# Kernel tuning notes

Measured on AMD Instinct MI355X. Metric: run time of the kernel, lower is better.

Reference implementation:

```python
import jax, jax.numpy as jnp
import numpy as np

HEAD_SIZE = 64
N_EMBD = 1024
BLOCK_SIZE = 2048


def setup_inputs() -> dict:
    key = jax.random.key(0)
    ks = jax.random.split(key, 7)
    B, T = 4, 2048
    s = 1.0 / np.sqrt(N_EMBD)
    return {
        "x": jax.random.normal(ks[0], (B, T, N_EMBD), dtype=jnp.float32),
        "Wq": jax.random.normal(ks[1], (N_EMBD, HEAD_SIZE), dtype=jnp.float32) * s,
        "bq": jnp.zeros((HEAD_SIZE,), dtype=jnp.float32),
        "Wk": jax.random.normal(ks[2], (N_EMBD, HEAD_SIZE), dtype=jnp.float32) * s,
        "bk": jnp.zeros((HEAD_SIZE,), dtype=jnp.float32),
        "Wv": jax.random.normal(ks[3], (N_EMBD, HEAD_SIZE), dtype=jnp.float32) * s,
        "bv": jnp.zeros((HEAD_SIZE,), dtype=jnp.float32),
    }


def reference(x, Wq, bq, Wk, bk, Wv, bv):
    # x: [B, T, n_embd]
    B, T, _ = x.shape
    q = x @ Wq + bq  # [B, T, H]
    k = x @ Wk + bk
    v = x @ Wv + bv
    # Faithful to source: divides by head_size**(-0.5) == multiplies by sqrt(head_size)
    scale = jnp.float32(HEAD_SIZE) ** 0.5
    scores = jnp.einsum("bqh,bkh->bqk", q, k) * scale  # [B, T, T]
    causal = jnp.tril(jnp.ones((T, T), dtype=bool))
    scores = jnp.where(causal, scores, -jnp.inf)
    attn = jax.nn.softmax(scores, axis=-1)  # dropout p=0.0 (eval)
    out = jnp.einsum("bqk,bkh->bqh", attn, v)  # [B, T, H]
    return out
```

## Files before the change

kernel.cpp:

```cpp
#include <hip/hip_runtime.h>
#include <math.h>

#define NE 1024
#define HS 64
#define TT 2048
#define QSC 11.541560327111707f

typedef __bf16    v8bf __attribute__((ext_vector_type(8)));
typedef _Float16  v8h  __attribute__((ext_vector_type(8)));
typedef float     v4f  __attribute__((ext_vector_type(4)));

#define MFMA_BF(a, b, c)  __builtin_amdgcn_mfma_f32_16x16x32_bf16((a), (b), (c), 0, 0, 0)
#define MFMA_F16(a, b, c) __builtin_amdgcn_mfma_f32_16x16x32_f16((a), (b), (c), 0, 0, 0)

__device__ __forceinline__ void gl_lds16(const void* g, void* l) {
    __builtin_amdgcn_global_load_lds(
        (const __attribute__((address_space(1))) unsigned int*)g,
        (__attribute__((address_space(3))) unsigned int*)l, 16, 0, 0);
}
__device__ __forceinline__ void gl_lds4(const void* g, void* l) {
    __builtin_amdgcn_global_load_lds(
        (const __attribute__((address_space(1))) unsigned int*)g,
        (__attribute__((address_space(3))) unsigned int*)l, 4, 0, 0);
}

#define SYNC_VM(imm) do {                                   \
    __asm__ __volatile__("" ::: "memory");                  \
    __builtin_amdgcn_s_waitcnt(imm);                        \
    __builtin_amdgcn_s_barrier();                           \
    __asm__ __volatile__("" ::: "memory");                  \
} while (0)
#define WAIT_VM8  0x0F78
#define WAIT_VM0  0x0F70

__global__ __launch_bounds__(256) void prep_w(
    const float* __restrict__ Wq, const float* __restrict__ Wk,
    const float* __restrict__ Wv, char* __restrict__ imgW)
{
    __shared__ float t[64][65];
    const int bx = blockIdx.x, by = blockIdx.y;
    const float* W = (by == 0) ? Wq : ((by == 1) ? Wk : Wv);
    const int tid = threadIdx.x;
    const int cc = tid & 63, r4 = tid >> 6;
    #pragma unroll
    for (int p = 0; p < 16; ++p) {
        const int k = p * 4 + r4;
        t[k][cc] = W[(size_t)(bx * 64 + k) * HS + cc];
    }
    __syncthreads();
    #pragma unroll
    for (int e = 0; e < 4; ++e) {
        const int chunk = tid + e * 256;
        const int s2   = chunk >> 9;
        const int rem  = chunk & 511;
        const int ctl  = rem >> 7;
        const int rem2 = rem & 127;
        const int pl   = rem2 >> 6;
        const int rem3 = rem2 & 63;
        const int c    = rem3 >> 2;
        const int p16  = rem3 & 3;
        const int kb   = s2 * 32 + ((p16 ^ (c & 3)) << 3);
        const int ncol = ctl * 16 + c;
        v8bf o;
        #pragma unroll
        for (int j = 0; j < 8; ++j) {
            const float v = t[kb + j][ncol];
            const __bf16 h = (__bf16)v;
            o[j] = pl ? (__bf16)(v - (float)h) : h;
        }
        *(v8bf*)(imgW + (size_t)(bx * 2 + s2) * 24576
                 + (by * 4 + ctl) * 2048 + pl * 1024 + c * 64 + p16 * 16) = o;
    }
}

__global__ __launch_bounds__(256, 2) void proj(
    const float* __restrict__ x, const char* __restrict__ imgW,
    const float* __restrict__ bq, const float* __restrict__ bk,
    const float* __restrict__ bv,
    _Float16* __restrict__ qh, _Float16* __restrict__ ql,
    _Float16* __restrict__ kf, _Float16* __restrict__ vt)
{
    __shared__ __align__(16) char sbuf[3][26624];

    const int tid = threadIdx.x, lane = tid & 63, cg = tid >> 6;
    const int quad = lane >> 4, l16 = lane & 15;
    const int m0 = blockIdx.x * 16;

    const int wv = cg;
    const int xr0 = wv * 4 + (lane >> 5);
    const int xr1 = xr0 + 2;
    const int xp  = (lane >> 3) & 3;
    const int xj  = lane & 7;
    const float* gx0 = x + (size_t)(m0 + xr0) * NE + ((xp ^ (xr0 & 3)) << 3) + xj;
    const float* gx1 = x + (size_t)(m0 + xr1) * NE + ((xp ^ (xr1 & 3)) << 3) + xj;
    const int xl0 = wv * 512 + (lane & 63) * 4;
    const int xl1 = xl0 + 256;
    const char* gw = imgW + (size_t)tid * 16;

    v4f acc[3];
    #pragma unroll
    for (int i = 0; i < 3; ++i) acc[i] = (v4f){0.f, 0.f, 0.f, 0.f};

    #define STAGE(ks, xb_)  do {                                          \
        gl_lds4(gx0 + (ks) * 32, (xb_) + xl0);                            \
        gl_lds4(gx1 + (ks) * 32, (xb_) + xl1);                            \
        const char* gws_ = gw + (size_t)(ks) * 24576;                     \
        _Pragma("unroll")                                                 \
        for (int j_ = 0; j_ < 6; ++j_)                                    \
            gl_lds16(gws_ + j_ * 4096, (xb_) + 2048 + tid * 16 + j_ * 4096); \
    } while (0)

    auto compute = [&](int ks) {
        const char* xb = sbuf[ks % 3];
        const char* wb = xb + 2048;
        const int rl = l16;
        const int pA = quad ^ (rl & 3);
        const float4 a0 = *(const float4*)(xb + rl * 128 + pA * 32);
        const float4 a1 = *(const float4*)(xb + rl * 128 + pA * 32 + 16);
        const float av[8] = {a0.x, a0.y, a0.z, a0.w, a1.x, a1.y, a1.z, a1.w};
        v8bf ah, al;
        #pragma unroll
        for (int i = 0; i < 8; ++i) {
            const __bf16 h = (__bf16)av[i];
            ah[i] = h;
            al[i] = (__bf16)(av[i] - (float)h);
        }
        const int wo = l16 * 64 + ((quad ^ (l16 & 3)) << 4);
        #pragma unroll
        for (int j = 0; j < 3; ++j) {
            const char* base = wb + (cg * 3 + j) * 2048 + wo;
            const v8bf bh = *(const v8bf*)(base);
            const v8bf bl = *(const v8bf*)(base + 1024);
            acc[j] = MFMA_BF(ah, bh, acc[j]);
            acc[j] = MFMA_BF(ah, bl, acc[j]);
            acc[j] = MFMA_BF(al, bh, acc[j]);
        }
    };

    STAGE(0, sbuf[0]);
    STAGE(1, sbuf[1]);
    for (int ks = 0; ks < 31; ++ks) {
        SYNC_VM(WAIT_VM8);
        if (ks + 2 < 32) STAGE(ks + 2, sbuf[(ks + 2) % 3]);
        compute(ks);
    }
    SYNC_VM(WAIT_VM0);
    compute(31);
    #undef STAGE

    #pragma unroll
    for (int j = 0; j < 3; ++j) {
        const int n = cg * 48 + j * 16 + l16;
        const float bias = (n < 64) ? bq[n] : ((n < 128) ? bk[n - 64] : bv[n - 128]);
        #pragma unroll
        for (int reg = 0; reg < 4; ++reg) {
            const int row = m0 + quad * 4 + reg;
            const float v = acc[j][reg] + bias;
            if (n < 64) {
                const float s = v * QSC;
                const _Float16 hh = (_Float16)s;
                qh[(size_t)row * HS + n] = hh;
                ql[(size_t)row * HS + n] = (_Float16)(s - (float)hh);
            } else if (n < 128) {
                kf[(size_t)row * HS + n - 64] = (_Float16)v;
            } else {
                const int b2 = row >> 11, tt = row & 2047, hc = n - 128;
                vt[((size_t)(b2 * HS + hc)) * TT + tt] = (_Float16)v;
            }
        }
    }
}

__global__ __launch_bounds__(512, 2) void attn(
    const _Float16* __restrict__ qh, const _Float16* __restrict__ ql,
    const _Float16* __restrict__ kf, const _Float16* __restrict__ vt,
    float* __restrict__ out)
{
    __shared__ __align__(16) char smem_raw[69632];
    _Float16* ps = (_Float16*)smem_raw;
    float*    os = (float*)smem_raw;
    __shared__ float sm[8][2][16], sl[8][2][16];

    const int tid = threadIdx.x, lane = tid & 63, w = tid >> 6;
    const int quad = lane >> 4, l16 = lane & 15;
    const int b = blockIdx.x & 3, pair = blockIdx.x >> 2;
    const int q0t[2] = {(127 - pair) * 16, pair * 16};
    const int ntk0 = (q0t[0] + 16 + 63) >> 6;
    const int ntk1 = (q0t[1] + 16 + 63) >> 6;
    const int total = ntk0 + ntk1;

    v8h Qh0[2], Qh1[2], Ql0[2], Ql1[2];
    #pragma unroll
    for (int t = 0; t < 2; ++t) {
        const size_t qrow = ((size_t)b * TT + q0t[t] + l16) * HS;
        Qh0[t] = *(const v8h*)(qh + qrow + quad * 8);
        Qh1[t] = *(const v8h*)(qh + qrow + 32 + quad * 8);
        Ql0[t] = *(const v8h*)(ql + qrow + quad * 8);
        Ql1[t] = *(const v8h*)(ql + qrow + 32 + quad * 8);
    }

    const v8h vones = {(_Float16)1.f, (_Float16)1.f, (_Float16)1.f, (_Float16)1.f,
                       (_Float16)1.f, (_Float16)1.f, (_Float16)1.f, (_Float16)1.f};

    float mr0[4] = {-3e38f, -3e38f, -3e38f, -3e38f};
    float mr1[4] = {-3e38f, -3e38f, -3e38f, -3e38f};
    v4f o0[4], o1[4], l40, l41;
    #pragma unroll
    for (int i = 0; i < 4; ++i) {
        o0[i] = (v4f){0.f, 0.f, 0.f, 0.f};
        o1[i] = (v4f){0.f, 0.f, 0.f, 0.f};
    }
    l40 = (v4f){0.f, 0.f, 0.f, 0.f};
    l41 = (v4f){0.f, 0.f, 0.f, 0.f};

    _Float16* pw = ps + w * (16 * 72);

    auto doChunk = [&](int j0, int q0c, int t,
                       float (&mrow)[4], v4f (&o)[4], v4f &o4) {
        v8h Kf[8], Vf[8];
        #pragma unroll
        for (int nt = 0; nt < 4; ++nt) {
            const size_t krow = ((size_t)b * TT + j0 + nt * 16 + l16) * HS;
            Kf[nt * 2]     = *(const v8h*)(kf + krow + quad * 8);
            Kf[nt * 2 + 1] = *(const v8h*)(kf + krow + 32 + quad * 8);
        }
        #pragma unroll
        for (int nt = 0; nt < 4; ++nt) {
            const size_t vrow = ((size_t)(b * HS + nt * 16 + l16)) * TT + j0;
            Vf[nt * 2]     = *(const v8h*)(vt + vrow + quad * 8);
            Vf[nt * 2 + 1] = *(const v8h*)(vt + vrow + 32 + quad * 8);
        }
        v4f s[4];
        #pragma unroll
        for (int i = 0; i < 4; ++i) s[i] = (v4f){0.f, 0.f, 0.f, 0.f};
        #pragma unroll
        for (int nt = 0; nt < 4; ++nt) {
            s[nt] = MFMA_F16(Qh0[t], Kf[nt * 2],     s[nt]);
            s[nt] = MFMA_F16(Qh1[t], Kf[nt * 2 + 1], s[nt]);
            s[nt] = MFMA_F16(Ql0[t], Kf[nt * 2],     s[nt]);
            s[nt] = MFMA_F16(Ql1[t], Kf[nt * 2 + 1], s[nt]);
        }
        const int irow = q0c + quad * 4;
        float mx[4] = {-3e38f, -3e38f, -3e38f, -3e38f};
        #pragma unroll
        for (int nt = 0; nt < 4; ++nt)
            #pragma unroll
            for (int reg = 0; reg < 4; ++reg) {
                if (j0 + nt * 16 + l16 > irow + reg) s[nt][reg] = -3e38f;
                mx[reg] = fmaxf(mx[reg], s[nt][reg]);
            }
        #pragma unroll
        for (int off = 8; off; off >>= 1)
            #pragma unroll
            for (int reg = 0; reg < 4; ++reg)
                mx[reg] = fmaxf(mx[reg], __shfl_xor(mx[reg], off));
        float al[4];
        #pragma unroll
        for (int reg = 0; reg < 4; ++reg) {
            const float mn = fmaxf(mrow[reg], mx[reg]);
            al[reg] = exp2f(mrow[reg] - mn);
            mrow[reg] = mn;
        }
        #pragma unroll
        for (int nt = 0; nt < 4; ++nt)
            #pragma unroll
            for (int reg = 0; reg < 4; ++reg) {
                const float p = (j0 + nt * 16 + l16 > irow + reg)
                                    ? 0.f : exp2f(s[nt][reg] - mrow[reg]);
                pw[(quad * 4 + reg) * 72 + nt * 16 + l16] = (_Float16)p;
            }
        #pragma unroll
        for (int nt = 0; nt < 4; ++nt)
            #pragma unroll
            for (int reg = 0; reg < 4; ++reg)
                o[nt][reg] *= al[reg];
        #pragma unroll
        for (int reg = 0; reg < 4; ++reg)
            o4[reg] *= al[reg];
        const v8h Pa0 = *(const v8h*)(pw + l16 * 72 + quad * 8);
        const v8h Pa1 = *(const v8h*)(pw + l16 * 72 + 32 + quad * 8);
        #pragma unroll
        for (int nt = 0; nt < 4; ++nt) {
            o[nt] = MFMA_F16(Pa0, Vf[nt * 2],     o[nt]);
            o[nt] = MFMA_F16(Pa1, Vf[nt * 2 + 1], o[nt]);
        }
        o4 = MFMA_F16(Pa0, vones, o4);
        o4 = MFMA_F16(Pa1, vones, o4);
    };

    for (int c = w; c < total; c += 8) {
        if (c < ntk0) doChunk(c * 64,          q0t[0], 0, mr0, o0, l40);
        else          doChunk((c - ntk0) * 64, q0t[1], 1, mr1, o1, l41);
    }

    if (l16 == 0) {
        #pragma unroll
        for (int reg = 0; reg < 4; ++reg) {
            sm[w][0][quad * 4 + reg] = mr0[reg];
            sl[w][0][quad * 4 + reg] = l40[reg];
            sm[w][1][quad * 4 + reg] = mr1[reg];
            sl[w][1][quad * 4 + reg] = l41[reg];
        }
    }
    __syncthreads();

    #pragma unroll
    for (int t = 0; t < 2; ++t) {
        float sc[4];
        #pragma unroll
        for (int reg = 0; reg < 4; ++reg) {
            const int r = quad * 4 + reg;
            float M = sm[0][t][r];
            #pragma unroll
            for (int i = 1; i < 8; ++i) M = fmaxf(M, sm[i][t][r]);
            const float mw = t ? mr1[reg] : mr0[reg];
            sc[reg] = exp2f(mw - M);
        }
        float* ow = os + (size_t)(w * 2 + t) * (16 * 68);
        #pragma unroll
        for (int nt = 0; nt < 4; ++nt)
            #pragma unroll
            for (int reg = 0; reg < 4; ++reg) {
                const v4f& oo = t ? o1[nt] : o0[nt];
                ow[(quad * 4 + reg) * 68 + nt * 16 + l16] = oo[reg] * sc[reg];
            }
    }
    __syncthreads();

    #pragma unroll
    for (int kk = 0; kk < 4; ++kk) {
        const int g = w * 4 + kk;
        const int t = g >> 4, m = g & 15;
        float M = sm[0][t][m];
        #pragma unroll
        for (int i = 1; i < 8; ++i) M = fmaxf(M, sm[i][t][m]);
        float L = 0.f, val = 0.f;
        #pragma unroll
        for (int i = 0; i < 8; ++i) {
            L   += sl[i][t][m] * exp2f(sm[i][t][m] - M);
            val += os[(size_t)(i * 2 + t) * (16 * 68) + m * 68 + lane];
        }
        out[((size_t)b * TT + q0t[t] + m) * HS + lane] = val / L;
    }
}

extern "C" void kernel_launch(void* const* d_in, const int* in_sizes, int n_in,
                              void* d_out, int out_size, void* d_ws, size_t ws_size,
                              hipStream_t stream)
{
    const float* x  = (const float*)d_in[0];
    const float* Wq = (const float*)d_in[1];
    const float* bq = (const float*)d_in[2];
    const float* Wk = (const float*)d_in[3];
    const float* bk = (const float*)d_in[4];
    const float* Wv = (const float*)d_in[5];
    const float* bv = (const float*)d_in[6];
    float* out = (float*)d_out;

    const int rows = in_sizes[0] / NE;
    char* p = (char*)d_ws;
    char* imgW = p;                           p += (size_t)32 * 24576;
    _Float16* qhb = (_Float16*)p;             p += (size_t)rows * HS * 2;
    _Float16* qlb = (_Float16*)p;             p += (size_t)rows * HS * 2;
    _Float16* kfb = (_Float16*)p;             p += (size_t)rows * HS * 2;
    _Float16* vtb = (_Float16*)p;             p += (size_t)rows * HS * 2;

    prep_w<<<dim3(16, 3), 256, 0, stream>>>(Wq, Wk, Wv, imgW);
    proj<<<rows / 16, 256, 0, stream>>>(x, imgW, bq, bk, bv,
                                        qhb, qlb, kfb, vtb);
    attn<<<rows / 32, 512, 0, stream>>>(qhb, qlb, kfb, vtb, out);
}
```

Measured before the change: 129.8 us.

## Retile projection blocks to 32 rows and prefetch next K chunk in attention

The projection kernel now gives each block 32 rows of x and half of the 192 output columns, loading x with 16-byte LDS-direct loads instead of 4-byte ones and shrinking the LDS stage buffers. Waves are split into two row tiles and two column groups. The attention kernel double-buffers K fragments in registers, loading the next chunk's K before computing the current one to hide global load latency. In exchange, x is fetched by two blocks per row tile and the attention loop uses more registers, which could lower occupancy.

```diff
diff --git a/kernel.cpp b/kernel.cpp
--- a/kernel.cpp
+++ b/kernel.cpp
@@ -17,11 +17,6 @@
     __builtin_amdgcn_global_load_lds(
         (const __attribute__((address_space(1))) unsigned int*)g,
         (__attribute__((address_space(3))) unsigned int*)l, 16, 0, 0);
-}
-__device__ __forceinline__ void gl_lds4(const void* g, void* l) {
-    __builtin_amdgcn_global_load_lds(
-        (const __attribute__((address_space(1))) unsigned int*)g,
-        (__attribute__((address_space(3))) unsigned int*)l, 4, 0, 0);
 }
 
 #define SYNC_VM(imm) do {                                   \
@@ -30,7 +25,7 @@
     __builtin_amdgcn_s_barrier();                           \
     __asm__ __volatile__("" ::: "memory");                  \
 } while (0)
-#define WAIT_VM8  0x0F78
+#define WAIT_VM4  0x0F74
 #define WAIT_VM0  0x0F70
 
 __global__ __launch_bounds__(256) void prep_w(
@@ -80,40 +75,40 @@
     _Float16* __restrict__ qh, _Float16* __restrict__ ql,
     _Float16* __restrict__ kf, _Float16* __restrict__ vt)
 {
-    __shared__ __align__(16) char sbuf[3][26624];
+    __shared__ __align__(16) char sbuf[3][16384];
 
     const int tid = threadIdx.x, lane = tid & 63, cg = tid >> 6;
     const int quad = lane >> 4, l16 = lane & 15;
-    const int m0 = blockIdx.x * 16;
-
-    const int wv = cg;
-    const int xr0 = wv * 4 + (lane >> 5);
-    const int xr1 = xr0 + 2;
-    const int xp  = (lane >> 3) & 3;
-    const int xj  = lane & 7;
-    const float* gx0 = x + (size_t)(m0 + xr0) * NE + ((xp ^ (xr0 & 3)) << 3) + xj;
-    const float* gx1 = x + (size_t)(m0 + xr1) * NE + ((xp ^ (xr1 & 3)) << 3) + xj;
-    const int xl0 = wv * 512 + (lane & 63) * 4;
-    const int xl1 = xl0 + 256;
-    const char* gw = imgW + (size_t)tid * 16;
+    const int bx = blockIdx.x;
+    const int m0 = (bx >> 1) * 32;
+    const int h  = bx & 1;
+
+    const int xrow = cg * 8 + (lane >> 3);
+    const int xp   = (lane >> 1) & 3;
+    const int xh   = lane & 1;
+    const float* gx = x + (size_t)(m0 + xrow) * NE
+                        + ((xp ^ (xrow & 3)) << 3) + (xh << 2);
+    const int xl = cg * 1024 + lane * 16;
+    const char* gw = imgW + (size_t)h * 12288 + (size_t)tid * 16;
 
     v4f acc[3];
     #pragma unroll
     for (int i = 0; i < 3; ++i) acc[i] = (v4f){0.f, 0.f, 0.f, 0.f};
 
     #define STAGE(ks, xb_)  do {                                          \
-        gl_lds4(gx0 + (ks) * 32, (xb_) + xl0);                            \
-        gl_lds4(gx1 + (ks) * 32, (xb_) + xl1);                            \
+        gl_lds16(gx + (ks) * 32, (xb_) + xl);                             \
         const char* gws_ = gw + (size_t)(ks) * 24576;                     \
         _Pragma("unroll")                                                 \
-        for (int j_ = 0; j_ < 6; ++j_)                                    \
-            gl_lds16(gws_ + j_ * 4096, (xb_) + 2048 + tid * 16 + j_ * 4096); \
+        for (int j_ = 0; j_ < 3; ++j_)                                    \
+            gl_lds16(gws_ + j_ * 4096, (xb_) + 4096 + tid * 16 + j_ * 4096); \
     } while (0)
 
     auto compute = [&](int ks) {
         const char* xb = sbuf[ks % 3];
-        const char* wb = xb + 2048;
-        const int rl = l16;
+        const char* wb = xb + 4096;
+        const int mt = cg >> 1;
+        const int wc = cg & 1;
+        const int rl = mt * 16 + l16;
         const int pA = quad ^ (rl & 3);
         const float4 a0 = *(const float4*)(xb + rl * 128 + pA * 32);
         const float4 a1 = *(const float4*)(xb + rl * 128 + pA * 32 + 16);
@@ -121,14 +116,14 @@
         v8bf ah, al;
         #pragma unroll
         for (int i = 0; i < 8; ++i) {
-            const __bf16 h = (__bf16)av[i];
-            ah[i] = h;
-            al[i] = (__bf16)(av[i] - (float)h);
+            const __bf16 hv = (__bf16)av[i];
+            ah[i] = hv;
+            al[i] = (__bf16)(av[i] - (float)hv);
         }
         const int wo = l16 * 64 + ((quad ^ (l16 & 3)) << 4);
         #pragma unroll
         for (int j = 0; j < 3; ++j) {
-            const char* base = wb + (cg * 3 + j) * 2048 + wo;
+            const char* base = wb + (wc * 3 + j) * 2048 + wo;
             const v8bf bh = *(const v8bf*)(base);
             const v8bf bl = *(const v8bf*)(base + 1024);
             acc[j] = MFMA_BF(ah, bh, acc[j]);
@@ -140,7 +135,7 @@
     STAGE(0, sbuf[0]);
     STAGE(1, sbuf[1]);
     for (int ks = 0; ks < 31; ++ks) {
-        SYNC_VM(WAIT_VM8);
+        SYNC_VM(WAIT_VM4);
         if (ks + 2 < 32) STAGE(ks + 2, sbuf[(ks + 2) % 3]);
         compute(ks);
     }
@@ -148,13 +143,14 @@
     compute(31);
     #undef STAGE
 
+    const int mt = cg >> 1, wc = cg & 1;
     #pragma unroll
     for (int j = 0; j < 3; ++j) {
-        const int n = cg * 48 + j * 16 + l16;
+        const int n = h * 96 + wc * 48 + j * 16 + l16;
         const float bias = (n < 64) ? bq[n] : ((n < 128) ? bk[n - 64] : bv[n - 128]);
         #pragma unroll
         for (int reg = 0; reg < 4; ++reg) {
-            const int row = m0 + quad * 4 + reg;
+            const int row = m0 + mt * 16 + quad * 4 + reg;
             const float v = acc[j][reg] + bias;
             if (n < 64) {
                 const float s = v * QSC;
@@ -215,15 +211,18 @@
 
     _Float16* pw = ps + w * (16 * 72);
 
-    auto doChunk = [&](int j0, int q0c, int t,
-                       float (&mrow)[4], v4f (&o)[4], v4f &o4) {
-        v8h Kf[8], Vf[8];
+    auto loadK = [&](int j0, v8h (&Kf)[8]) {
         #pragma unroll
         for (int nt = 0; nt < 4; ++nt) {
             const size_t krow = ((size_t)b * TT + j0 + nt * 16 + l16) * HS;
             Kf[nt * 2]     = *(const v8h*)(kf + krow + quad * 8);
             Kf[nt * 2 + 1] = *(const v8h*)(kf + krow + 32 + quad * 8);
         }
+    };
+
+    auto doChunk = [&](int j0, int q0c, int t, const v8h (&Kf)[8],
+                       float (&mrow)[4], v4f (&o)[4], v4f &o4) {
+        v8h Vf[8];
         #pragma unroll
         for (int nt = 0; nt < 4; ++nt) {
             const size_t vrow = ((size_t)(b * HS + nt * 16 + l16)) * TT + j0;
@@ -288,9 +287,25 @@
         o4 = MFMA_F16(Pa1, vones, o4);
     };
 
-    for (int c = w; c < total; c += 8) {
-        if (c < ntk0) doChunk(c * 64,          q0t[0], 0, mr0, o0, l40);
-        else          doChunk((c - ntk0) * 64, q0t[1], 1, mr1, o1, l41);
+    auto jof = [&](int c) { return (c < ntk0) ? c * 64 : (c - ntk0) * 64; };
+
+    {
+        v8h KA[8], KB[8];
+        int c = w;
+        loadK(jof(c), KA);
+        while (true) {
+            int cn = c + 8;
+            if (cn < total) loadK(jof(cn), KB);
+            if (c < ntk0) doChunk(c * 64,          q0t[0], 0, KA, mr0, o0, l40);
+            else          doChunk((c - ntk0) * 64, q0t[1], 1, KA, mr1, o1, l41);
+            if (cn >= total) break;
+            c = cn; cn = c + 8;
+            if (cn < total) loadK(jof(cn), KA);
+            if (c < ntk0) doChunk(c * 64,          q0t[0], 0, KB, mr0, o0, l40);
+            else          doChunk((c - ntk0) * 64, q0t[1], 1, KB, mr1, o1, l41);
+            if (cn >= total) break;
+            c = cn;
+        }
     }
 
     if (l16 == 0) {
```

Measured after the change: 127.8 us. About the same (-1.5%).
